# Optimization experiments

Measured on AMD Instinct MI355X. Metric: run time of the kernel, lower is better.

Reference implementation:

```python
import jax, jax.numpy as jnp
import numpy as np

NUM_NODES = 100000
NUM_EDGES = 1600000
NUM_GRAPHS = 64
IN_DIM = 128
HID = 128
OUT_DIM = 256
NUM_LAYERS = 5
BN_EPS = 1e-5


def _bn(t, gamma, beta):
    # BatchNorm1d forward with batch statistics (biased variance), as in train mode
    m = jnp.mean(t, axis=0)
    v = jnp.var(t, axis=0)
    return gamma * (t - m) * jax.lax.rsqrt(v + BN_EPS) + beta


def setup_inputs() -> dict:
    key = jax.random.key(0)
    ks = jax.random.split(key, 16)
    x = jax.random.normal(ks[0], (NUM_NODES, IN_DIM), dtype=jnp.float32)
    edge_index = jax.random.randint(ks[1], (2, NUM_EDGES), 0, NUM_NODES, dtype=jnp.int64)
    batch = jnp.sort(jax.random.randint(ks[2], (NUM_NODES,), 0, NUM_GRAPHS, dtype=jnp.int64))
    s1 = 1.0 / np.sqrt(IN_DIM)
    s2 = 1.0 / np.sqrt(HID)
    # stacked per-layer GIN MLP params: Linear(HID,HID) -> BN -> ReLU -> Linear(HID,HID)
    w1 = jax.random.normal(ks[3], (NUM_LAYERS, HID, HID), dtype=jnp.float32) * s1
    b1 = jnp.zeros((NUM_LAYERS, HID), dtype=jnp.float32)
    gamma1 = jnp.ones((NUM_LAYERS, HID), dtype=jnp.float32)
    beta1 = jnp.zeros((NUM_LAYERS, HID), dtype=jnp.float32)
    w2 = jax.random.normal(ks[4], (NUM_LAYERS, HID, HID), dtype=jnp.float32) * s2
    b2 = jnp.zeros((NUM_LAYERS, HID), dtype=jnp.float32)
    # outer per-layer BatchNorm after each GINConv
    gamma_bn = jnp.ones((NUM_LAYERS, HID), dtype=jnp.float32)
    beta_bn = jnp.zeros((NUM_LAYERS, HID), dtype=jnp.float32)
    # output projection Linear(HID, OUT_DIM)
    wp = jax.random.normal(ks[5], (HID, OUT_DIM), dtype=jnp.float32) * s2
    bp = jnp.zeros((OUT_DIM,), dtype=jnp.float32)
    return {"x": x, "edge_index": edge_index, "batch": batch,
            "w1": w1, "b1": b1, "gamma1": gamma1, "beta1": beta1,
            "w2": w2, "b2": b2, "gamma_bn": gamma_bn, "beta_bn": beta_bn,
            "wp": wp, "bp": bp}


def reference(x, edge_index, batch, w1, b1, gamma1, beta1, w2, b2, gamma_bn, beta_bn, wp, bp):
    src, dst = edge_index[0], edge_index[1]
    h = x
    for i in range(NUM_LAYERS):
        # GINConv, eps=0: mlp((1+eps)*h + sum_{j in N(i)} h_j)
        agg = jax.ops.segment_sum(h[src], dst, num_segments=NUM_NODES)
        z = h + agg
        t = _bn(z @ w1[i] + b1[i], gamma1[i], beta1[i])
        t = jax.nn.relu(t)
        t = t @ w2[i] + b2[i]
        # outer BatchNorm + ReLU (dropout p handled as identity in eval)
        t = jax.nn.relu(_bn(t, gamma_bn[i], beta_bn[i]))
        h = h + t  # residual (dims always match)
    node_emb = h
    # global mean pool per graph
    sums = jax.ops.segment_sum(h, batch, num_segments=NUM_GRAPHS)
    counts = jax.ops.segment_sum(jnp.ones((NUM_NODES,), dtype=h.dtype), batch, num_segments=NUM_GRAPHS)
    pooled = sums / jnp.maximum(counts, 1.0)[:, None]
    graph_emb = pooled @ wp + bp
    return graph_emb, node_emb
```

## Files before the change

### kernel.cpp

```cpp
#include <hip/hip_runtime.h>

#define NNODES 100000
#define NEDGES 1600000
#define NGRAPHS 64
#define HID 128
#define OUTD 256
#define NLAYERS 5
#define BN_EPS 1e-5f
#define NBUCK 196
#define BUCKCAP 9216
#define FILL_BLOCKS 391
#define NREP 8

typedef __attribute__((ext_vector_type(8))) short short8;
typedef __attribute__((ext_vector_type(4))) float f32x4;

__device__ inline unsigned short f2b(float f) {
    union { float f; unsigned int u; } a; a.f = f;
    unsigned int u = a.u;
    return (unsigned short)((u + 0x7FFF + ((u >> 16) & 1)) >> 16);
}
__device__ inline float b2f(unsigned short b) {
    union { unsigned int u; float f; } a; a.u = ((unsigned int)b) << 16;
    return a.f;
}

__global__ void k_init(const float* __restrict__ x, float* __restrict__ h,
                       ushort* __restrict__ hb) {
    int i = blockIdx.x * 256 + threadIdx.x;
    float4 v = ((const float4*)x)[i];
    ((float4*)h)[i] = v;
    ushort4 o;
    o.x = f2b(v.x); o.y = f2b(v.y); o.z = f2b(v.z); o.w = f2b(v.w);
    ((ushort4*)hb)[i] = o;
}

__global__ void k_bcur0(int* __restrict__ bcur) {
    int t = threadIdx.x;
    if (t < NBUCK) bcur[t] = t * BUCKCAP;
}

__global__ __launch_bounds__(256) void k_fill1(
    const int* __restrict__ srcv, const int* __restrict__ dstv,
    int* __restrict__ bcur, unsigned int* __restrict__ packed) {
    __shared__ int hist[NBUCK];
    __shared__ int base[NBUCK];
    int tid = threadIdx.x;
    int e0 = blockIdx.x * 4096;
    for (int i = tid; i < NBUCK; i += 256) hist[i] = 0;
    __syncthreads();
#pragma unroll
    for (int i = 0; i < 16; i++) {
        int e = e0 + i * 256 + tid;
        if (e < NEDGES) atomicAdd(&hist[dstv[e] >> 9], 1);
    }
    __syncthreads();
    for (int i = tid; i < NBUCK; i += 256) {
        int c = hist[i];
        base[i] = c ? atomicAdd(&bcur[i], c) : 0;
        hist[i] = 0;
    }
    __syncthreads();
#pragma unroll
    for (int i = 0; i < 16; i++) {
        int e = e0 + i * 256 + tid;
        if (e < NEDGES) {
            int d = dstv[e];
            int b = d >> 9;
            int r = atomicAdd(&hist[b], 1);
            packed[base[b] + r] = ((unsigned int)srcv[e] << 9) | (unsigned int)(d & 511);
        }
    }
}

__global__ __launch_bounds__(256) void k_fill2(
    const unsigned int* __restrict__ packed, const int* __restrict__ bcur,
    int2* __restrict__ off2, int* __restrict__ adj) {
    __shared__ int deg[512];
    __shared__ int cur[512];
    int tid = threadIdx.x;
    int b = blockIdx.x;
    int base = b * BUCKCAP;
    int cnt = bcur[b] - base;
    deg[tid] = 0; deg[tid + 256] = 0;
    __syncthreads();
    for (int i = tid; i < cnt; i += 256)
        atomicAdd(&deg[packed[base + i] & 511], 1);
    __syncthreads();
    cur[tid] = deg[tid]; cur[tid + 256] = deg[tid + 256];
    __syncthreads();
    for (int o = 1; o < 512; o <<= 1) {
        int u0 = (tid >= o) ? cur[tid - o] : 0;
        int u1 = (tid + 256 >= o) ? cur[tid + 256 - o] : 0;
        __syncthreads();
        cur[tid] += u0; cur[tid + 256] += u1;
        __syncthreads();
    }
    int nbase = b * 512;
#pragma unroll
    for (int i = 0; i < 2; i++) {
        int t = tid + i * 256;
        int st = base + cur[t] - deg[t];
        int n = nbase + t;
        if (n < NNODES) off2[n] = make_int2(st, st + deg[t]);
    }
    __syncthreads();
#pragma unroll
    for (int i = 0; i < 2; i++) {
        int t = tid + i * 256;
        cur[t] = base + cur[t] - deg[t];
    }
    __syncthreads();
    for (int i = tid; i < cnt; i += 256) {
        unsigned int p = packed[base + i];
        int r = atomicAdd(&cur[p & 511], 1);
        adj[r] = (int)(p >> 9);
    }
}

__global__ void k_wt(const float* __restrict__ w1, const float* __restrict__ w2,
                     unsigned short* __restrict__ WT) {
    int t = blockIdx.x * 256 + threadIdx.x;
    int mat = t >> 14;
    int rem = t & 16383;
    int k = rem >> 7, n = rem & 127;
    const float* src = (mat < 5) ? &w1[(size_t)mat * 16384] : &w2[(size_t)(mat - 5) * 16384];
    WT[(size_t)mat * 16384 + n * 128 + k] = f2b(src[k * 128 + n]);
}

__global__ void k_agg(const ushort* __restrict__ hb, const int2* __restrict__ off2,
                      const int* __restrict__ adj, ushort* __restrict__ zb) {
    int tid = threadIdx.x;
    int node = blockIdx.x * 8 + (tid >> 5);
    int d4 = tid & 31;
    const ushort4* hb4 = (const ushort4*)hb;
    ushort4 sv = hb4[(size_t)node * 32 + d4];
    float4 v = make_float4(b2f(sv.x), b2f(sv.y), b2f(sv.z), b2f(sv.w));
    int2 oo = off2[node];
    int e = oo.x, e1 = oo.y;
    for (; e + 8 <= e1; e += 8) {
        int s[8]; ushort4 u[8];
#pragma unroll
        for (int j = 0; j < 8; j++) s[j] = adj[e + j];
#pragma unroll
        for (int j = 0; j < 8; j++) u[j] = hb4[(size_t)s[j] * 32 + d4];
#pragma unroll
        for (int j = 0; j < 8; j++) {
            v.x += b2f(u[j].x); v.y += b2f(u[j].y);
            v.z += b2f(u[j].z); v.w += b2f(u[j].w);
        }
    }
    for (; e + 4 <= e1; e += 4) {
        int s0 = adj[e], s1 = adj[e + 1], s2 = adj[e + 2], s3 = adj[e + 3];
        ushort4 u0 = hb4[(size_t)s0 * 32 + d4];
        ushort4 u1 = hb4[(size_t)s1 * 32 + d4];
        ushort4 u2 = hb4[(size_t)s2 * 32 + d4];
        ushort4 u3 = hb4[(size_t)s3 * 32 + d4];
        v.x += (b2f(u0.x) + b2f(u1.x)) + (b2f(u2.x) + b2f(u3.x));
        v.y += (b2f(u0.y) + b2f(u1.y)) + (b2f(u2.y) + b2f(u3.y));
        v.z += (b2f(u0.z) + b2f(u1.z)) + (b2f(u2.z) + b2f(u3.z));
        v.w += (b2f(u0.w) + b2f(u1.w)) + (b2f(u2.w) + b2f(u3.w));
    }
    for (; e < e1; e++) {
        int s = adj[e];
        ushort4 u = hb4[(size_t)s * 32 + d4];
        v.x += b2f(u.x); v.y += b2f(u.y); v.z += b2f(u.z); v.w += b2f(u.w);
    }
    ushort4 o;
    o.x = f2b(v.x); o.y = f2b(v.y); o.z = f2b(v.z); o.w = f2b(v.w);
    ((ushort4*)zb)[(size_t)node * 32 + d4] = o;
}

__global__ __launch_bounds__(256) void k_gemm1(
    const ushort* __restrict__ A, const unsigned short* __restrict__ WT,
    const float* __restrict__ bias, ushort* __restrict__ C,
    float* __restrict__ stats) {
    __shared__ float lstat[256];
    int tid = threadIdx.x;
    int wave = tid >> 6;
    int lane = tid & 63;
    int q = lane >> 4;
    int l16 = lane & 15;
    int rowbase = blockIdx.x * 128 + wave * 32;

    f32x4 acc[2][8];
#pragma unroll
    for (int rt = 0; rt < 2; rt++)
#pragma unroll
        for (int nt = 0; nt < 8; nt++) acc[rt][nt] = (f32x4){0.f, 0.f, 0.f, 0.f};

    for (int kc = 0; kc < 4; kc++) {
        int k0 = kc * 32 + q * 8;
        short8 bf[8];
#pragma unroll
        for (int nt = 0; nt < 8; nt++)
            bf[nt] = *(const short8*)&WT[(size_t)(nt * 16 + l16) * 128 + k0];
#pragma unroll
        for (int rt = 0; rt < 2; rt++) {
            int row = rowbase + rt * 16 + l16;
            if (row >= NNODES) row = NNODES - 1;
            short8 av = *(const short8*)&A[(size_t)row * 128 + k0];
#pragma unroll
            for (int nt = 0; nt < 8; nt++)
                acc[rt][nt] = __builtin_amdgcn_mfma_f32_16x16x32_bf16(
                    av, bf[nt], acc[rt][nt], 0, 0, 0);
        }
    }

    lstat[tid] = 0.f;
    __syncthreads();
#pragma unroll
    for (int nt = 0; nt < 8; nt++) {
        float b = bias[nt * 16 + l16];
        float csum = 0.f, csq = 0.f;
#pragma unroll
        for (int rt = 0; rt < 2; rt++) {
            int rb = rowbase + rt * 16 + q * 4;
#pragma unroll
            for (int r = 0; r < 4; r++) {
                int row = rb + r;
                if (row < NNODES) {
                    float v = acc[rt][nt][r] + b;
                    C[(size_t)row * 128 + nt * 16 + l16] = f2b(v);
                    csum += v; csq += v * v;
                }
            }
        }
        csum += __shfl_xor(csum, 16, 64); csq += __shfl_xor(csq, 16, 64);
        csum += __shfl_xor(csum, 32, 64); csq += __shfl_xor(csq, 32, 64);
        if (q == 0) {
            atomicAdd(&lstat[nt * 16 + l16], csum);
            atomicAdd(&lstat[128 + nt * 16 + l16], csq);
        }
    }
    __syncthreads();
    atomicAdd(&stats[((blockIdx.x & (NREP - 1)) << 8) + tid], lstat[tid]);
}

__global__ __launch_bounds__(256) void k_gemm2(
    const ushort* __restrict__ A, const unsigned short* __restrict__ WT,
    const float* __restrict__ bias, ushort* __restrict__ C,
    const float* __restrict__ statsIn, const float* __restrict__ gamma,
    const float* __restrict__ beta, float* __restrict__ stats) {
    __shared__ float lstat[256];
    __shared__ float s_sc[128], s_sh[128];
    int tid = threadIdx.x;
    if (tid < 128) {
        float s = 0.f, qq = 0.f;
#pragma unroll
        for (int r = 0; r < NREP; r++) {
            s  += statsIn[r * 256 + tid];
            qq += statsIn[r * 256 + 128 + tid];
        }
        float m = s * (1.f / NNODES);
        float var = qq * (1.f / NNODES) - m * m;
        float sc = gamma[tid] * rsqrtf(var + BN_EPS);
        s_sc[tid] = sc;
        s_sh[tid] = beta[tid] - m * sc;
    }
    __syncthreads();

    int wave = tid >> 6;
    int lane = tid & 63;
    int q = lane >> 4;
    int l16 = lane & 15;
    int rowbase = blockIdx.x * 128 + wave * 32;

    f32x4 acc[2][8];
#pragma unroll
    for (int rt = 0; rt < 2; rt++)
#pragma unroll
        for (int nt = 0; nt < 8; nt++) acc[rt][nt] = (f32x4){0.f, 0.f, 0.f, 0.f};

    for (int kc = 0; kc < 4; kc++) {
        int k0 = kc * 32 + q * 8;
        short8 bf[8];
#pragma unroll
        for (int nt = 0; nt < 8; nt++)
            bf[nt] = *(const short8*)&WT[(size_t)(nt * 16 + l16) * 128 + k0];

        float4 s0 = *(const float4*)&s_sc[k0];
        float4 s1 = *(const float4*)&s_sc[k0 + 4];
        float4 t0 = *(const float4*)&s_sh[k0];
        float4 t1 = *(const float4*)&s_sh[k0 + 4];
        float scl[8] = {s0.x, s0.y, s0.z, s0.w, s1.x, s1.y, s1.z, s1.w};
        float shf[8] = {t0.x, t0.y, t0.z, t0.w, t1.x, t1.y, t1.z, t1.w};
#pragma unroll
        for (int rt = 0; rt < 2; rt++) {
            int row = rowbase + rt * 16 + l16;
            if (row >= NNODES) row = NNODES - 1;
            union { short8 s; unsigned short u[8]; } in, cv;
            in.s = *(const short8*)&A[(size_t)row * 128 + k0];
#pragma unroll
            for (int j = 0; j < 8; j++) {
                float f = fmaxf(b2f(in.u[j]) * scl[j] + shf[j], 0.f);
                cv.u[j] = f2b(f);
            }
#pragma unroll
            for (int nt = 0; nt < 8; nt++)
                acc[rt][nt] = __builtin_amdgcn_mfma_f32_16x16x32_bf16(
                    cv.s, bf[nt], acc[rt][nt], 0, 0, 0);
        }
    }

    lstat[tid] = 0.f;
    __syncthreads();
#pragma unroll
    for (int nt = 0; nt < 8; nt++) {
        float b = bias[nt * 16 + l16];
        float csum = 0.f, csq = 0.f;
#pragma unroll
        for (int rt = 0; rt < 2; rt++) {
            int rb = rowbase + rt * 16 + q * 4;
#pragma unroll
            for (int r = 0; r < 4; r++) {
                int row = rb + r;
                if (row < NNODES) {
                    float v = acc[rt][nt][r] + b;
                    C[(size_t)row * 128 + nt * 16 + l16] = f2b(v);
                    csum += v; csq += v * v;
                }
            }
        }
        csum += __shfl_xor(csum, 16, 64); csq += __shfl_xor(csq, 16, 64);
        csum += __shfl_xor(csum, 32, 64); csq += __shfl_xor(csq, 32, 64);
        if (q == 0) {
            atomicAdd(&lstat[nt * 16 + l16], csum);
            atomicAdd(&lstat[128 + nt * 16 + l16], csq);
        }
    }
    __syncthreads();
    atomicAdd(&stats[((blockIdx.x & (NREP - 1)) << 8) + tid], lstat[tid]);
}

__global__ void k_resid(float* __restrict__ h, ushort* __restrict__ hb,
                        const ushort* __restrict__ t2b,
                        const float* __restrict__ statsIn,
                        const float* __restrict__ gamma, const float* __restrict__ beta) {
    __shared__ float s_sc[128], s_sh[128];
    int tid = threadIdx.x;
    if (tid < 128) {
        float s = 0.f, qq = 0.f;
#pragma unroll
        for (int r = 0; r < NREP; r++) {
            s  += statsIn[r * 256 + tid];
            qq += statsIn[r * 256 + 128 + tid];
        }
        float m = s * (1.f / NNODES);
        float var = qq * (1.f / NNODES) - m * m;
        float sc = gamma[tid] * rsqrtf(var + BN_EPS);
        s_sc[tid] = sc;
        s_sh[tid] = beta[tid] - m * sc;
    }
    __syncthreads();
    int i = blockIdx.x * 256 + tid;
    int c4 = (i & 31) * 4;
    float4 sc = *(const float4*)&s_sc[c4];
    float4 sh = *(const float4*)&s_sh[c4];
    ushort4 t = ((const ushort4*)t2b)[i];
    float4 hv = ((float4*)h)[i];
    hv.x += fmaxf(b2f(t.x) * sc.x + sh.x, 0.f);
    hv.y += fmaxf(b2f(t.y) * sc.y + sh.y, 0.f);
    hv.z += fmaxf(b2f(t.z) * sc.z + sh.z, 0.f);
    hv.w += fmaxf(b2f(t.w) * sc.w + sh.w, 0.f);
    ((float4*)h)[i] = hv;
    ushort4 o;
    o.x = f2b(hv.x); o.y = f2b(hv.y); o.z = f2b(hv.z); o.w = f2b(hv.w);
    ((ushort4*)hb)[i] = o;
}

__global__ void k_counts(const int* __restrict__ batch, float* __restrict__ cnt) {
    int g = threadIdx.x;
    if (g >= NGRAPHS) return;
    auto lb = [&](int key) {
        int lo = 0, hi = NNODES;
        while (lo < hi) {
            int mid = (lo + hi) >> 1;
            if (batch[mid] < key) lo = mid + 1; else hi = mid;
        }
        return lo;
    };
    cnt[g] = (float)(lb(g + 1) - lb(g));
}

__global__ void k_pool(const float* __restrict__ h, const int* __restrict__ batch,
                       float* __restrict__ pooled) {
    __shared__ float4 red[256];
    int t = threadIdx.x;
    int d4 = t & 31, sub = t >> 5;
    int n0 = blockIdx.x * 128;
    if (n0 >= NNODES) return;
    int n1 = n0 + 128; if (n1 > NNODES) n1 = NNODES;
    int glo = batch[n0], ghi = batch[n1 - 1];
    for (int g = glo; g <= ghi; g++) {
        float4 acc = make_float4(0.f, 0.f, 0.f, 0.f);
        for (int r = n0 + sub; r < n1; r += 8) {
            if (batch[r] == g) {
                float4 v = ((const float4*)h)[(size_t)r * 32 + d4];
                acc.x += v.x; acc.y += v.y; acc.z += v.z; acc.w += v.w;
            }
        }
        red[t] = acc;
        __syncthreads();
        if (sub < 4) {
            float4 o = red[t + 128];
            red[t].x += o.x; red[t].y += o.y; red[t].z += o.z; red[t].w += o.w;
        }
        __syncthreads();
        if (sub < 2) {
            float4 o = red[t + 64];
            red[t].x += o.x; red[t].y += o.y; red[t].z += o.z; red[t].w += o.w;
        }
        __syncthreads();
        if (sub == 0) {
            float4 o = red[t + 32];
            float4 a = red[t];
            a.x += o.x; a.y += o.y; a.z += o.z; a.w += o.w;
            atomicAdd(&pooled[g * 128 + d4 * 4 + 0], a.x);
            atomicAdd(&pooled[g * 128 + d4 * 4 + 1], a.y);
            atomicAdd(&pooled[g * 128 + d4 * 4 + 2], a.z);
            atomicAdd(&pooled[g * 128 + d4 * 4 + 3], a.w);
        }
        __syncthreads();
    }
}

__global__ void k_proj(const float* __restrict__ pooled, const float* __restrict__ cnt,
                       const float* __restrict__ wp, const float* __restrict__ bp,
                       float* __restrict__ out) {
    __shared__ float prow[128];
    int g = blockIdx.x, c = threadIdx.x;
    if (c < 128) prow[c] = pooled[g * 128 + c] / fmaxf(cnt[g], 1.f);
    __syncthreads();
    float acc = bp[c];
    for (int k = 0; k < 128; k++) acc += prow[k] * wp[k * 256 + c];
    out[g * 256 + c] = acc;
}

extern "C" void kernel_launch(void* const* d_in, const int* in_sizes, int n_in,
                              void* d_out, int out_size, void* d_ws, size_t ws_size,
                              hipStream_t stream) {
    const float* x    = (const float*)d_in[0];
    const int*   eidx = (const int*)d_in[1];
    const int*   batch= (const int*)d_in[2];
    const float* w1   = (const float*)d_in[3];
    const float* b1   = (const float*)d_in[4];
    const float* g1   = (const float*)d_in[5];
    const float* be1  = (const float*)d_in[6];
    const float* w2   = (const float*)d_in[7];
    const float* b2   = (const float*)d_in[8];
    const float* gbn  = (const float*)d_in[9];
    const float* bbn  = (const float*)d_in[10];
    const float* wp   = (const float*)d_in[11];
    const float* bp   = (const float*)d_in[12];

    float* out  = (float*)d_out;
    float* gemb = out;
    float* h    = out + (size_t)NGRAPHS * OUTD;

    char* w = (char*)d_ws;
    ushort* hb   = (ushort*)w; w += (size_t)NNODES * 128 * 2;
    ushort* zb   = (ushort*)w; w += (size_t)NNODES * 128 * 2;
    ushort* tb   = (ushort*)w; w += (size_t)NNODES * 128 * 2;
    ushort* t2b  = (ushort*)w; w += (size_t)NNODES * 128 * 2;
    int2*  off2  = (int2*)w;  w += (size_t)NNODES * 8;
    int*   adj   = (int*)w;   w += (size_t)NBUCK * BUCKCAP * 4;
    unsigned short* WT = (unsigned short*)w; w += (size_t)10 * 16384 * 2;
    int*   bcur  = (int*)w;   w += 256 * 4;
    float* statsAll = (float*)w; w += (size_t)10 * NREP * 256 * 4;
    float* pooled= (float*)w; w += (size_t)NGRAPHS * HID * 4;
    float* gcnt  = (float*)w; w += NGRAPHS * 4;

    unsigned int* packed = (unsigned int*)tb;

    const int* srcv = eidx;
    const int* dstv = eidx + NEDGES;

    k_init<<<NNODES * 32 / 256, 256, 0, stream>>>(x, h, hb);

    k_wt<<<640, 256, 0, stream>>>(w1, w2, WT);

    hipMemsetAsync(statsAll, 0,
                   ((size_t)10 * NREP * 256 + NGRAPHS * HID + NGRAPHS) * 4, stream);

    k_bcur0<<<1, 256, 0, stream>>>(bcur);
    k_fill1<<<FILL_BLOCKS, 256, 0, stream>>>(srcv, dstv, bcur, packed);
    k_fill2<<<NBUCK, 256, 0, stream>>>(packed, bcur, off2, adj);

    const int GB = (NNODES + 127) / 128;
    for (int i = 0; i < NLAYERS; i++) {
        float* st1 = statsAll + (size_t)(2 * i) * NREP * 256;
        float* st2 = statsAll + (size_t)(2 * i + 1) * NREP * 256;
        k_agg<<<NNODES / 8, 256, 0, stream>>>(hb, off2, adj, zb);
        k_gemm1<<<GB, 256, 0, stream>>>(
            zb, WT + (size_t)i * 16384, b1 + i * HID, tb, st1);
        k_gemm2<<<GB, 256, 0, stream>>>(
            tb, WT + (size_t)(5 + i) * 16384, b2 + i * HID, t2b,
            st1, g1 + i * HID, be1 + i * HID, st2);
        k_resid<<<NNODES * 128 / 4 / 256, 256, 0, stream>>>(
            h, hb, t2b, st2, gbn + i * HID, bbn + i * HID);
    }

    k_counts<<<1, 64, 0, stream>>>(batch, gcnt);
    k_pool<<<(NNODES + 127) / 128, 256, 0, stream>>>(h, batch, pooled);
    k_proj<<<NGRAPHS, 256, 0, stream>>>(pooled, gcnt, wp, bp, gemb);
}
```

Baseline: 1.062 ms.

## Fuse neighbor aggregation into first GEMM via LDS staging; fold counts into projection

Merges the gather-sum aggregation kernel into the first MLP GEMM. Each block aggregates its 128 nodes into a padded LDS tile, then runs MFMA on it directly, so the bf16 z buffer never goes through global memory. The graph-count binary search also moves into the projection kernel, which removes one launch. The risk is lower parallelism in the gather phase: 782 blocks with a large LDS footprint, against 12500 small blocks before, so there is less latency hiding for the random neighbor reads.

```diff
diff --git a/kernel.cpp b/kernel.cpp
--- a/kernel.cpp
+++ b/kernel.cpp
@@ -11,6 +11,7 @@
 #define BUCKCAP 9216
 #define FILL_BLOCKS 391
 #define NREP 8
+#define ZSTR 136
 
 typedef __attribute__((ext_vector_type(8))) short short8;
 typedef __attribute__((ext_vector_type(4))) float f32x4;
@@ -128,60 +129,69 @@
     WT[(size_t)mat * 16384 + n * 128 + k] = f2b(src[k * 128 + n]);
 }
 
-__global__ void k_agg(const ushort* __restrict__ hb, const int2* __restrict__ off2,
-                      const int* __restrict__ adj, ushort* __restrict__ zb) {
-    int tid = threadIdx.x;
-    int node = blockIdx.x * 8 + (tid >> 5);
-    int d4 = tid & 31;
-    const ushort4* hb4 = (const ushort4*)hb;
-    ushort4 sv = hb4[(size_t)node * 32 + d4];
-    float4 v = make_float4(b2f(sv.x), b2f(sv.y), b2f(sv.z), b2f(sv.w));
-    int2 oo = off2[node];
-    int e = oo.x, e1 = oo.y;
-    for (; e + 8 <= e1; e += 8) {
-        int s[8]; ushort4 u[8];
-#pragma unroll
-        for (int j = 0; j < 8; j++) s[j] = adj[e + j];
-#pragma unroll
-        for (int j = 0; j < 8; j++) u[j] = hb4[(size_t)s[j] * 32 + d4];
-#pragma unroll
-        for (int j = 0; j < 8; j++) {
-            v.x += b2f(u[j].x); v.y += b2f(u[j].y);
-            v.z += b2f(u[j].z); v.w += b2f(u[j].w);
-        }
-    }
-    for (; e + 4 <= e1; e += 4) {
-        int s0 = adj[e], s1 = adj[e + 1], s2 = adj[e + 2], s3 = adj[e + 3];
-        ushort4 u0 = hb4[(size_t)s0 * 32 + d4];
-        ushort4 u1 = hb4[(size_t)s1 * 32 + d4];
-        ushort4 u2 = hb4[(size_t)s2 * 32 + d4];
-        ushort4 u3 = hb4[(size_t)s3 * 32 + d4];
-        v.x += (b2f(u0.x) + b2f(u1.x)) + (b2f(u2.x) + b2f(u3.x));
-        v.y += (b2f(u0.y) + b2f(u1.y)) + (b2f(u2.y) + b2f(u3.y));
-        v.z += (b2f(u0.z) + b2f(u1.z)) + (b2f(u2.z) + b2f(u3.z));
-        v.w += (b2f(u0.w) + b2f(u1.w)) + (b2f(u2.w) + b2f(u3.w));
-    }
-    for (; e < e1; e++) {
-        int s = adj[e];
-        ushort4 u = hb4[(size_t)s * 32 + d4];
-        v.x += b2f(u.x); v.y += b2f(u.y); v.z += b2f(u.z); v.w += b2f(u.w);
-    }
-    ushort4 o;
-    o.x = f2b(v.x); o.y = f2b(v.y); o.z = f2b(v.z); o.w = f2b(v.w);
-    ((ushort4*)zb)[(size_t)node * 32 + d4] = o;
-}
-
-__global__ __launch_bounds__(256) void k_gemm1(
-    const ushort* __restrict__ A, const unsigned short* __restrict__ WT,
+__global__ __launch_bounds__(256) void k_aggemm1(
+    const ushort* __restrict__ hb, const int2* __restrict__ off2,
+    const int* __restrict__ adj, const unsigned short* __restrict__ WT,
     const float* __restrict__ bias, ushort* __restrict__ C,
     float* __restrict__ stats) {
+    __shared__ ushort zs[128 * ZSTR];
     __shared__ float lstat[256];
     int tid = threadIdx.x;
+    int nbase = blockIdx.x * 128;
+    const ushort4* hb4 = (const ushort4*)hb;
+
+    int d4 = tid & 31;
+    int sub = tid >> 5;
+    for (int it = 0; it < 16; it++) {
+        int lr = it * 8 + sub;
+        int node = nbase + lr;
+        ushort4 o;
+        if (node < NNODES) {
+            ushort4 sv = hb4[(size_t)node * 32 + d4];
+            float4 v = make_float4(b2f(sv.x), b2f(sv.y), b2f(sv.z), b2f(sv.w));
+            int2 oo = off2[node];
+            int e = oo.x, e1 = oo.y;
+            for (; e + 8 <= e1; e += 8) {
+                int s[8]; ushort4 u[8];
+#pragma unroll
+                for (int j = 0; j < 8; j++) s[j] = adj[e + j];
+#pragma unroll
+                for (int j = 0; j < 8; j++) u[j] = hb4[(size_t)s[j] * 32 + d4];
+#pragma unroll
+                for (int j = 0; j < 8; j++) {
+                    v.x += b2f(u[j].x); v.y += b2f(u[j].y);
+                    v.z += b2f(u[j].z); v.w += b2f(u[j].w);
+                }
+            }
+            for (; e + 4 <= e1; e += 4) {
+                int s0 = adj[e], s1 = adj[e + 1], s2 = adj[e + 2], s3 = adj[e + 3];
+                ushort4 u0 = hb4[(size_t)s0 * 32 + d4];
+                ushort4 u1 = hb4[(size_t)s1 * 32 + d4];
+                ushort4 u2 = hb4[(size_t)s2 * 32 + d4];
+                ushort4 u3 = hb4[(size_t)s3 * 32 + d4];
+                v.x += (b2f(u0.x) + b2f(u1.x)) + (b2f(u2.x) + b2f(u3.x));
+                v.y += (b2f(u0.y) + b2f(u1.y)) + (b2f(u2.y) + b2f(u3.y));
+                v.z += (b2f(u0.z) + b2f(u1.z)) + (b2f(u2.z) + b2f(u3.z));
+                v.w += (b2f(u0.w) + b2f(u1.w)) + (b2f(u2.w) + b2f(u3.w));
+            }
+            for (; e < e1; e++) {
+                int s = adj[e];
+                ushort4 u = hb4[(size_t)s * 32 + d4];
+                v.x += b2f(u.x); v.y += b2f(u.y); v.z += b2f(u.z); v.w += b2f(u.w);
+            }
+            o.x = f2b(v.x); o.y = f2b(v.y); o.z = f2b(v.z); o.w = f2b(v.w);
+        } else {
+            o = make_ushort4(0, 0, 0, 0);
+        }
+        *(ushort4*)&zs[lr * ZSTR + d4 * 4] = o;
+    }
+    __syncthreads();
+
     int wave = tid >> 6;
     int lane = tid & 63;
     int q = lane >> 4;
     int l16 = lane & 15;
-    int rowbase = blockIdx.x * 128 + wave * 32;
+    int lrow0 = wave * 32;
 
     f32x4 acc[2][8];
 #pragma unroll
@@ -197,9 +207,7 @@
             bf[nt] = *(const short8*)&WT[(size_t)(nt * 16 + l16) * 128 + k0];
 #pragma unroll
         for (int rt = 0; rt < 2; rt++) {
-            int row = rowbase + rt * 16 + l16;
-            if (row >= NNODES) row = NNODES - 1;
-            short8 av = *(const short8*)&A[(size_t)row * 128 + k0];
+            short8 av = *(const short8*)&zs[(lrow0 + rt * 16 + l16) * ZSTR + k0];
 #pragma unroll
             for (int nt = 0; nt < 8; nt++)
                 acc[rt][nt] = __builtin_amdgcn_mfma_f32_16x16x32_bf16(
@@ -209,6 +217,7 @@
 
     lstat[tid] = 0.f;
     __syncthreads();
+    int rowbase = nbase + lrow0;
 #pragma unroll
     for (int nt = 0; nt < 8; nt++) {
         float b = bias[nt * 16 + l16];
@@ -367,20 +376,6 @@
     ushort4 o;
     o.x = f2b(hv.x); o.y = f2b(hv.y); o.z = f2b(hv.z); o.w = f2b(hv.w);
     ((ushort4*)hb)[i] = o;
-}
-
-__global__ void k_counts(const int* __restrict__ batch, float* __restrict__ cnt) {
-    int g = threadIdx.x;
-    if (g >= NGRAPHS) return;
-    auto lb = [&](int key) {
-        int lo = 0, hi = NNODES;
-        while (lo < hi) {
-            int mid = (lo + hi) >> 1;
-            if (batch[mid] < key) lo = mid + 1; else hi = mid;
-        }
-        return lo;
-    };
-    cnt[g] = (float)(lb(g + 1) - lb(g));
 }
 
 __global__ void k_pool(const float* __restrict__ h, const int* __restrict__ batch,
@@ -425,12 +420,26 @@
     }
 }
 
-__global__ void k_proj(const float* __restrict__ pooled, const float* __restrict__ cnt,
+__global__ void k_proj(const float* __restrict__ pooled, const int* __restrict__ batch,
                        const float* __restrict__ wp, const float* __restrict__ bp,
                        float* __restrict__ out) {
     __shared__ float prow[128];
+    __shared__ float inv_cnt;
     int g = blockIdx.x, c = threadIdx.x;
-    if (c < 128) prow[c] = pooled[g * 128 + c] / fmaxf(cnt[g], 1.f);
+    if (c == 0) {
+        auto lb = [&](int key) {
+            int lo = 0, hi = NNODES;
+            while (lo < hi) {
+                int mid = (lo + hi) >> 1;
+                if (batch[mid] < key) lo = mid + 1; else hi = mid;
+            }
+            return lo;
+        };
+        float cnt = (float)(lb(g + 1) - lb(g));
+        inv_cnt = 1.f / fmaxf(cnt, 1.f);
+    }
+    __syncthreads();
+    if (c < 128) prow[c] = pooled[g * 128 + c] * inv_cnt;
     __syncthreads();
     float acc = bp[c];
     for (int k = 0; k < 128; k++) acc += prow[k] * wp[k * 256 + c];
@@ -460,7 +469,6 @@
 
     char* w = (char*)d_ws;
     ushort* hb   = (ushort*)w; w += (size_t)NNODES * 128 * 2;
-    ushort* zb   = (ushort*)w; w += (size_t)NNODES * 128 * 2;
     ushort* tb   = (ushort*)w; w += (size_t)NNODES * 128 * 2;
     ushort* t2b  = (ushort*)w; w += (size_t)NNODES * 128 * 2;
     int2*  off2  = (int2*)w;  w += (size_t)NNODES * 8;
@@ -469,7 +477,6 @@
     int*   bcur  = (int*)w;   w += 256 * 4;
     float* statsAll = (float*)w; w += (size_t)10 * NREP * 256 * 4;
     float* pooled= (float*)w; w += (size_t)NGRAPHS * HID * 4;
-    float* gcnt  = (float*)w; w += NGRAPHS * 4;
 
     unsigned int* packed = (unsigned int*)tb;
 
@@ -481,7 +488,7 @@
     k_wt<<<640, 256, 0, stream>>>(w1, w2, WT);
 
     hipMemsetAsync(statsAll, 0,
-                   ((size_t)10 * NREP * 256 + NGRAPHS * HID + NGRAPHS) * 4, stream);
+                   ((size_t)10 * NREP * 256 + NGRAPHS * HID) * 4, stream);
 
     k_bcur0<<<1, 256, 0, stream>>>(bcur);
     k_fill1<<<FILL_BLOCKS, 256, 0, stream>>>(srcv, dstv, bcur, packed);
@@ -491,9 +498,8 @@
     for (int i = 0; i < NLAYERS; i++) {
         float* st1 = statsAll + (size_t)(2 * i) * NREP * 256;
         float* st2 = statsAll + (size_t)(2 * i + 1) * NREP * 256;
-        k_agg<<<NNODES / 8, 256, 0, stream>>>(hb, off2, adj, zb);
-        k_gemm1<<<GB, 256, 0, stream>>>(
-            zb, WT + (size_t)i * 16384, b1 + i * HID, tb, st1);
+        k_aggemm1<<<GB, 256, 0, stream>>>(
+            hb, off2, adj, WT + (size_t)i * 16384, b1 + i * HID, tb, st1);
         k_gemm2<<<GB, 256, 0, stream>>>(
             tb, WT + (size_t)(5 + i) * 16384, b2 + i * HID, t2b,
             st1, g1 + i * HID, be1 + i * HID, st2);
@@ -501,7 +507,6 @@
             h, hb, t2b, st2, gbn + i * HID, bbn + i * HID);
     }
 
-    k_counts<<<1, 64, 0, stream>>>(batch, gcnt);
     k_pool<<<(NNODES + 127) / 128, 256, 0, stream>>>(h, batch, pooled);
-    k_proj<<<NGRAPHS, 256, 0, stream>>>(pooled, gcnt, wp, bp, gemb);
-}
+    k_proj<<<NGRAPHS, 256, 0, stream>>>(pooled, batch, wp, bp, gemb);
+}
```

Result: slower. 1.344 ms (+26.6%).
